# Kernel optimization log

Measured on AMD Instinct MI355X. Metric: run time of the kernel, lower is better.

The kernel has to match this reference:

```python
import jax, jax.numpy as jnp
import numpy as np
import math

N_HEADS = 32
N_KV_HEADS = 8
HEAD_DIM = 64
THETA = 10000.0
NEG_INF = -1e9


def _rope_cos_sin(seq_len, dim, dtype=jnp.float32):
    # freqs over even indices, matching torch.arange(0, dim, 2)/dim
    freqs = 1.0 / (THETA ** (jnp.arange(0, dim, 2, dtype=jnp.float32) / dim))  # [dim/2]
    angles = jnp.arange(seq_len, dtype=jnp.float32)[:, None] * freqs[None, :]  # [S, dim/2]
    return jnp.cos(angles).astype(dtype), jnp.sin(angles).astype(dtype)


def _apply_rope(x, cos, sin):
    # x: [B, S, H, D]; pairs (x[...,2i], x[...,2i+1]) rotated as complex numbers
    xr = x[..., 0::2]
    xi = x[..., 1::2]
    # broadcast cos/sin [S, D/2] -> [1, S, 1, D/2]
    c = cos[None, :, None, :]
    s = sin[None, :, None, :]
    or_ = xr * c - xi * s
    oi_ = xr * s + xi * c
    # interleave back: [..., D/2, 2] -> [..., D]
    return jnp.stack([or_, oi_], axis=-1).reshape(x.shape)


def setup_inputs() -> dict:
    key = jax.random.key(0)
    ks = jax.random.split(key, 5)
    B, S, D = 2, 2048, 2048
    KV_D = N_KV_HEADS * HEAD_DIM
    x = jax.random.normal(ks[0], (B, S, D), dtype=jnp.float32)
    sc = 1.0 / math.sqrt(D)
    wq = jax.random.normal(ks[1], (D, D), dtype=jnp.float32) * sc
    wk = jax.random.normal(ks[2], (D, KV_D), dtype=jnp.float32) * sc
    wv = jax.random.normal(ks[3], (D, KV_D), dtype=jnp.float32) * sc
    wo = jax.random.normal(ks[4], (D, D), dtype=jnp.float32) * sc
    # additive causal mask [1, 1, S, S]
    causal = jnp.tril(jnp.ones((S, S), dtype=bool))
    mask = jnp.where(causal, 0.0, NEG_INF).astype(jnp.float32)[None, None]
    return {"x": x, "mask": mask, "wq": wq, "wk": wk, "wv": wv, "wo": wo}


def reference(x, mask, wq, wk, wv, wo):
    B, S, D = x.shape
    n_rep = N_HEADS // N_KV_HEADS
    q = (x @ wq).reshape(B, S, N_HEADS, HEAD_DIM)
    k = (x @ wk).reshape(B, S, N_KV_HEADS, HEAD_DIM)
    v = (x @ wv).reshape(B, S, N_KV_HEADS, HEAD_DIM)
    cos, sin = _rope_cos_sin(S, HEAD_DIM)
    q = _apply_rope(q, cos, sin)
    k = _apply_rope(k, cos, sin)
    # GQA: repeat_interleave kv heads along head dim
    k = jnp.repeat(k, n_rep, axis=2)  # [B, S, H, D]
    v = jnp.repeat(v, n_rep, axis=2)
    scores = jnp.einsum("bqhd,bkhd->bhqk", q, k) / math.sqrt(HEAD_DIM)
    scores = scores + mask
    probs = jax.nn.softmax(scores.astype(jnp.float32), axis=-1).astype(q.dtype)
    out = jnp.einsum("bhqk,bkhd->bqhd", probs, v).reshape(B, S, N_HEADS * HEAD_DIM)
    return out @ wo
```

## Files before the change

### kernel.cpp

```cpp
#include <hip/hip_runtime.h>
#include <hip/hip_bf16.h>


#define S_LEN 2048
#define BATCH 2
#define D_MODEL 2048
#define NH 32
#define NKV 8
#define HD 64
#define KV_D (NKV * HD)
#define QKV_N (D_MODEL + 2 * KV_D)

typedef __attribute__((ext_vector_type(8))) short short8;
typedef __attribute__((ext_vector_type(4))) float float4v;

typedef __attribute__((address_space(1))) const unsigned int gu32;
typedef __attribute__((address_space(3))) unsigned int lu32;

#if __has_builtin(__builtin_amdgcn_exp2f)
#define PEXP(x) __builtin_amdgcn_exp2f(x)
#else
#define PEXP(x) __expf((x) * 0.69314718f)
#endif
#define QSCALE 0.18033688f

__device__ __forceinline__ float bf2f(unsigned short u) {
    unsigned x = ((unsigned)u) << 16;
    return __builtin_bit_cast(float, x);
}
__device__ __forceinline__ unsigned short f2bf(float f) {
    unsigned u = __builtin_bit_cast(unsigned, f);
    unsigned r = (u + 0x7fffu + ((u >> 16) & 1u)) >> 16;
    return (unsigned short)r;
}
__device__ __forceinline__ unsigned short f2bf_fast(float f) {
    return (unsigned short)((__builtin_bit_cast(unsigned, f) + 0x8000u) >> 16);
}

__global__ void cast_f32_bf16(const float* __restrict__ in,
                              unsigned short* __restrict__ out, long n) {
    long i = ((long)blockIdx.x * 256 + threadIdx.x) * 4;
    if (i + 3 >= n) return;
    const float4v v = *(const float4v*)&in[i];
    unsigned short o[4];
    o[0] = f2bf(v[0]); o[1] = f2bf(v[1]); o[2] = f2bf(v[2]); o[3] = f2bf(v[3]);
    *(__attribute__((ext_vector_type(4))) short*)&out[i] =
        *(__attribute__((ext_vector_type(4))) short*)o;
}

__global__ __launch_bounds__(256) void wtrans(const float* __restrict__ in,
                                              unsigned short* __restrict__ out,
                                              int K, int N) {
    __shared__ unsigned short t[32 * 33];
    const int nb = blockIdx.x * 32, kb = blockIdx.y * 32;
    const int c = threadIdx.x & 31, rr = threadIdx.x >> 5;
#pragma unroll
    for (int it = 0; it < 4; ++it) {
        int r = it * 8 + rr;
        t[c * 33 + r] = f2bf(in[(long)(kb + r) * N + nb + c]);
    }
    __syncthreads();
#pragma unroll
    for (int it = 0; it < 4; ++it) {
        int r = it * 8 + rr;
        out[(long)(nb + r) * K + kb + c] = t[r * 33 + c];
    }
}

template <int TM, bool F32OUT>
__global__ __launch_bounds__(256, TM == 64 ? 4 : 3)
void gemm_sw(const unsigned short* __restrict__ A,
             const unsigned short* __restrict__ BT,
             void* __restrict__ Cv, int M, int N, int K) {
    __shared__ unsigned short As[TM * 64];
    __shared__ unsigned short Bs[128 * 64];
    const int tid = threadIdx.x;
    const int wid = tid >> 6, lane = tid & 63;
    const int l15 = lane & 15, quad = lane >> 4;
    const int wm = (wid >> 1) * (TM / 2), wn = (wid & 1) * 64;
    const int row0 = blockIdx.x * TM, col0 = blockIdx.y * 128;
    constexpr int MI = TM / 32;

    float4v acc[MI][4];
    float4v z;
    z[0] = z[1] = z[2] = z[3] = 0.0f;
    for (int mi = 0; mi < MI; ++mi)
        for (int ni = 0; ni < 4; ++ni) acc[mi][ni] = z;

    const int r_ld = lane >> 3;
    const int swz_ld = ((lane & 7) ^ (lane >> 3)) * 8;
    const int sw = l15 & 7;

    for (int kb = 0; kb < K; kb += 64) {
        __syncthreads();
#pragma unroll
        for (int c = 0; c < 4; ++c) {
            int chunk = c * 4 + wid;
            int r = chunk * 8 + r_ld;
            __builtin_amdgcn_global_load_lds(
                (gu32*)&BT[(long)(col0 + r) * K + kb + swz_ld],
                (lu32*)&Bs[chunk * 512], 16, 0, 0);
            if (c < MI)
                __builtin_amdgcn_global_load_lds(
                    (gu32*)&A[(long)(row0 + r) * K + kb + swz_ld],
                    (lu32*)&As[chunk * 512], 16, 0, 0);
        }
        __syncthreads();
#pragma unroll
        for (int kk = 0; kk < 64; kk += 32) {
            short8 af[MI], bf[4];
#pragma unroll
            for (int i = 0; i < MI; ++i)
                af[i] = *(const short8*)
                    &As[(wm + i * 16 + l15) * 64 + ((((kk >> 3) + quad) ^ sw) << 3)];
#pragma unroll
            for (int i = 0; i < 4; ++i)
                bf[i] = *(const short8*)
                    &Bs[(wn + i * 16 + l15) * 64 + ((((kk >> 3) + quad) ^ sw) << 3)];
#pragma unroll
            for (int mi = 0; mi < MI; ++mi)
#pragma unroll
                for (int ni = 0; ni < 4; ++ni)
                    acc[mi][ni] = __builtin_amdgcn_mfma_f32_16x16x32_bf16(
                        af[mi], bf[ni], acc[mi][ni], 0, 0, 0);
        }
    }
#pragma unroll
    for (int mi = 0; mi < MI; ++mi)
#pragma unroll
        for (int ni = 0; ni < 4; ++ni)
#pragma unroll
            for (int r = 0; r < 4; ++r) {
                int m = row0 + wm + mi * 16 + quad * 4 + r;
                int n = col0 + wn + ni * 16 + l15;
                if (F32OUT)
                    ((float*)Cv)[(long)m * N + n] = acc[mi][ni][r];
                else
                    ((unsigned short*)Cv)[(long)m * N + n] = f2bf(acc[mi][ni][r]);
            }
}

__global__ __launch_bounds__(256) void rope2(unsigned short* __restrict__ qkv) {
    const int i = threadIdx.x & 31;
    const int row = blockIdx.x * 8 + (threadIdx.x >> 5);
    const int s = row & (S_LEN - 1);
    float freq = __expf(-0.28782313f * (float)i);
    float ang = (float)s * freq;
    float c = cosf(ang), sn = sinf(ang);
    unsigned* p = (unsigned*)qkv + ((long)row * QKV_N + 2 * i) / 2;
#pragma unroll
    for (int head = 0; head < 40; ++head) {
        const float qs = (head < 32) ? QSCALE : 1.0f;
        unsigned v = p[head * 32];
        float xr = bf2f((unsigned short)(v & 0xffff));
        float xi = bf2f((unsigned short)(v >> 16));
        unsigned short lo = f2bf((xr * c - xi * sn) * qs);
        unsigned short hi = f2bf((xr * sn + xi * c) * qs);
        p[head * 32] = (unsigned)lo | ((unsigned)hi << 16);
    }
}

__global__ __launch_bounds__(256) void vtrans(const unsigned short* __restrict__ qkv,
                                              unsigned short* __restrict__ Vt) {
    __shared__ unsigned t[64 * 33];
    const int st = blockIdx.x * 64, kh = blockIdx.y, b = blockIdx.z;
    const int tid = threadIdx.x;
    {
        const int r2 = tid >> 3, dbase = (tid & 7) * 8;
        const unsigned short* src =
            qkv + ((long)(b * S_LEN + st + 2 * r2)) * QKV_N + D_MODEL + KV_D + kh * HD + dbase;
        short8 lo = *(const short8*)src;
        short8 hi = *(const short8*)(src + QKV_N);
#pragma unroll
        for (int j = 0; j < 8; ++j)
            t[(dbase + j) * 33 + r2] =
                (unsigned)(unsigned short)lo[j] | ((unsigned)(unsigned short)hi[j] << 16);
    }
    __syncthreads();
    {
        const int d = tid >> 2, sb = (tid & 3) * 8;
        unsigned short o[16];
#pragma unroll
        for (int jj = 0; jj < 8; ++jj) {
            unsigned v = t[d * 33 + sb + jj];
            o[2 * jj] = (unsigned short)(v & 0xffff);
            o[2 * jj + 1] = (unsigned short)(v >> 16);
        }
        unsigned short* dst =
            Vt + ((long)((b * 8 + kh) * 64 + d)) * S_LEN + st + sb * 2;
        *(short8*)dst = *(short8*)&o[0];
        *(short8*)(dst + 8) = *(short8*)&o[8];
    }
}

__global__ __launch_bounds__(512, 4) void flash5(const unsigned short* __restrict__ qkv,
                                                 const unsigned short* __restrict__ Vt,
                                                 unsigned short* __restrict__ O) {
    __shared__ unsigned short Ks[2][64 * 64];
    __shared__ unsigned short Vs[2][64 * 64];
    __shared__ unsigned short Ps[8][16 * 72];

    const int tid = threadIdx.x, w = tid >> 6, lane = tid & 63;
    const int l15 = lane & 15, quad = lane >> 4;
    const int h = blockIdx.y, b = blockIdx.z;
    const int kh = h >> 2, bkh = b * 8 + kh;
    const int qtA = blockIdx.x;

    const int r_loc = lane >> 3;
    const int row_g = w * 8 + r_loc;
    const int swz_c = ((lane & 7) ^ r_loc) * 8;
    const unsigned short* Kg =
        qkv + (long)b * S_LEN * QKV_N + D_MODEL + kh * HD + swz_c;
    const unsigned short* Vg = Vt + ((long)bkh * 64 + row_g) * S_LEN + swz_c;
    const int sw = l15 & 7;

    float4v z;
    z[0] = z[1] = z[2] = z[3] = 0.0f;

    for (int tsel = 0; tsel < 2; ++tsel) {
        const int qt = tsel ? (15 - qtA) : qtA;
        const int m0 = qt * 128;
        const int row_w = m0 + w * 16;

        short8 aq[2];
        {
            const long qrow = ((long)(b * S_LEN) + row_w + l15) * QKV_N + h * HD;
            aq[0] = *(const short8*)&qkv[qrow + quad * 8];
            aq[1] = *(const short8*)&qkv[qrow + 32 + quad * 8];
        }

        float4v oacc[4];
        float lp[4];
#pragma unroll
        for (int nt = 0; nt < 4; ++nt) oacc[nt] = z;
#pragma unroll
        for (int r = 0; r < 4; ++r) lp[r] = 0.0f;

        const int nkt = 2 * qt + 2;

        __builtin_amdgcn_global_load_lds((gu32*)&Kg[(long)row_g * QKV_N],
                                         (lu32*)&Ks[0][w * 512], 16, 0, 0);
        __builtin_amdgcn_global_load_lds((gu32*)&Vg[0],
                                         (lu32*)&Vs[0][w * 512], 16, 0, 0);
        __syncthreads();

        for (int kti = 0; kti < nkt; ++kti) {
            const int k0 = kti * 64;
            const int cur = kti & 1;

            if (kti + 1 < nkt) {
                __builtin_amdgcn_global_load_lds(
                    (gu32*)&Kg[(long)(k0 + 64 + row_g) * QKV_N],
                    (lu32*)&Ks[cur ^ 1][w * 512], 16, 0, 0);
                __builtin_amdgcn_global_load_lds(
                    (gu32*)&Vg[k0 + 64],
                    (lu32*)&Vs[cur ^ 1][w * 512], 16, 0, 0);
            }

            if (row_w + 15 >= k0) {
                const bool maskband = (kti >= 2 * qt);

#pragma unroll
                for (int nt = 0; nt < 4; ++nt) {
                    const int rb = (nt * 16 + l15) * 64;
                    short8 bk0 = *(const short8*)&Ks[cur][rb + ((quad ^ sw) << 3)];
                    short8 bk1 = *(const short8*)&Ks[cur][rb + (((quad + 4) ^ sw) << 3)];
                    __builtin_amdgcn_s_setprio(1);
                    float4v s = __builtin_amdgcn_mfma_f32_16x16x32_bf16(aq[0], bk0, z, 0, 0, 0);
                    s = __builtin_amdgcn_mfma_f32_16x16x32_bf16(aq[1], bk1, s, 0, 0, 0);
                    __builtin_amdgcn_s_setprio(0);
#pragma unroll
                    for (int r = 0; r < 4; ++r) {
                        const int qidx = row_w + quad * 4 + r;
                        float v = s[r];
                        if (maskband && (k0 + nt * 16 + l15 > qidx)) v = -1e4f;
                        float p = PEXP(v);
                        lp[r] += p;
                        Ps[w][(quad * 4 + r) * 72 + nt * 16 + l15] = f2bf_fast(p);
                    }
                }

                short8 ap0 = *(const short8*)&Ps[w][l15 * 72 + quad * 8];
                short8 ap1 = *(const short8*)&Ps[w][l15 * 72 + 32 + quad * 8];
                __builtin_amdgcn_s_setprio(1);
#pragma unroll
                for (int nt = 0; nt < 4; ++nt) {
                    const int rb = (nt * 16 + l15) * 64;
                    short8 bv0 = *(const short8*)&Vs[cur][rb + ((quad ^ sw) << 3)];
                    short8 bv1 = *(const short8*)&Vs[cur][rb + (((quad + 4) ^ sw) << 3)];
                    oacc[nt] = __builtin_amdgcn_mfma_f32_16x16x32_bf16(ap0, bv0, oacc[nt], 0, 0, 0);
                    oacc[nt] = __builtin_amdgcn_mfma_f32_16x16x32_bf16(ap1, bv1, oacc[nt], 0, 0, 0);
                }
                __builtin_amdgcn_s_setprio(0);
            }
            __syncthreads();
        }

#pragma unroll
        for (int r = 0; r < 4; ++r) {
            float l = lp[r];
#pragma unroll
            for (int off = 1; off < 16; off <<= 1) l += __shfl_xor(l, off);
            float inv = 1.0f / l;
            int m = row_w + quad * 4 + r;
            long orow = ((long)(b * S_LEN) + m) * D_MODEL + h * HD;
#pragma unroll
            for (int nt = 0; nt < 4; ++nt)
                O[orow + nt * 16 + l15] = f2bf(oacc[nt][r] * inv);
        }
    }
}

extern "C" void kernel_launch(void* const* d_in, const int* in_sizes, int n_in,
                              void* d_out, int out_size, void* d_ws, size_t ws_size,
                              hipStream_t stream) {
    const float* x  = (const float*)d_in[0];
    const float* wq = (const float*)d_in[n_in - 4];
    const float* wk = (const float*)d_in[n_in - 3];
    const float* wv = (const float*)d_in[n_in - 2];
    const float* wo = (const float*)d_in[n_in - 1];
    float* out = (float*)d_out;

    unsigned short* ws    = (unsigned short*)d_ws;
    unsigned short* xb    = ws;
    unsigned short* Obuf  = ws;
    unsigned short* qkv   = xb + (long)BATCH * S_LEN * D_MODEL;
    unsigned short* woT   = qkv + (long)BATCH * S_LEN * QKV_N;
    unsigned short* wqkvT = woT + (long)D_MODEL * D_MODEL;
    unsigned short* Vt    = wqkvT;

    const int M = BATCH * S_LEN;
    const long xn = (long)M * D_MODEL;

    cast_f32_bf16<<<(int)(xn / 4 / 256), 256, 0, stream>>>(x, xb, xn);

    wtrans<<<dim3(D_MODEL / 32, D_MODEL / 32), 256, 0, stream>>>(wq, wqkvT, D_MODEL, D_MODEL);
    wtrans<<<dim3(KV_D / 32, D_MODEL / 32), 256, 0, stream>>>(wk, wqkvT + (long)D_MODEL * D_MODEL, D_MODEL, KV_D);
    wtrans<<<dim3(KV_D / 32, D_MODEL / 32), 256, 0, stream>>>(wv, wqkvT + (long)(D_MODEL + KV_D) * D_MODEL, D_MODEL, KV_D);
    wtrans<<<dim3(D_MODEL / 32, D_MODEL / 32), 256, 0, stream>>>(wo, woT, D_MODEL, D_MODEL);

    gemm_sw<128, false><<<dim3(M / 128, QKV_N / 128), 256, 0, stream>>>(
        xb, wqkvT, qkv, M, QKV_N, D_MODEL);

    rope2<<<M / 8, 256, 0, stream>>>(qkv);

    vtrans<<<dim3(S_LEN / 64, NKV, BATCH), 256, 0, stream>>>(qkv, Vt);

    flash5<<<dim3(8, NH, BATCH), 512, 0, stream>>>(qkv, Vt, Obuf);

    gemm_sw<64, true><<<dim3(M / 64, D_MODEL / 128), 256, 0, stream>>>(
        Obuf, woT, out, M, D_MODEL, D_MODEL);
}
```

Baseline: 313.2 us.

## Rewrite attention kernel with 32x32 MFMA and register-resident P

Replaces the flash attention kernel with a 4-wave variant that uses 32x32x16 bf16 MFMA. It computes S^T so the probabilities stay in registers and are repacked with cvt_pk_bf16 and permlane32 swaps, which removes the LDS round-trip for P. Each block now handles one query tile picked by a fixed permutation table, instead of pairing tiles for causal balance, and the grid doubles. The output is staged through LDS for coalesced 16-byte stores. It relies on gfx950-specific instructions and adds more accumulator register pressure.

```diff
diff --git a/kernel.cpp b/kernel.cpp
--- a/kernel.cpp
+++ b/kernel.cpp
@@ -13,6 +13,8 @@
 
 typedef __attribute__((ext_vector_type(8))) short short8;
 typedef __attribute__((ext_vector_type(4))) float float4v;
+typedef __attribute__((ext_vector_type(16))) float f32x16;
+typedef __attribute__((ext_vector_type(2))) unsigned uint2v;
 
 typedef __attribute__((address_space(1))) const unsigned int gu32;
 typedef __attribute__((address_space(3))) unsigned int lu32;
@@ -33,8 +35,26 @@
     unsigned r = (u + 0x7fffu + ((u >> 16) & 1u)) >> 16;
     return (unsigned short)r;
 }
-__device__ __forceinline__ unsigned short f2bf_fast(float f) {
-    return (unsigned short)((__builtin_bit_cast(unsigned, f) + 0x8000u) >> 16);
+
+__device__ __forceinline__ unsigned cvt_pk_bf16(float a, float b) {
+    unsigned r;
+    asm("v_cvt_pk_bf16_f32 %0, %1, %2" : "=v"(r) : "v"(a), "v"(b));
+    return r;
+}
+
+__device__ __forceinline__ void pl32swap(unsigned a, unsigned b,
+                                         unsigned& x, unsigned& y) {
+#if __has_builtin(__builtin_amdgcn_permlane32_swap)
+    uint2v r = __builtin_amdgcn_permlane32_swap(a, b, false, false);
+    x = r[0];
+    y = r[1];
+#else
+    unsigned pa = (unsigned)__shfl_xor((int)a, 32);
+    unsigned pb = (unsigned)__shfl_xor((int)b, 32);
+    bool lo = (threadIdx.x & 63) < 32;
+    x = lo ? a : pb;
+    y = lo ? pa : b;
+#endif
 }
 
 __global__ void cast_f32_bf16(const float* __restrict__ in,
@@ -193,122 +213,139 @@
     }
 }
 
-__global__ __launch_bounds__(512, 4) void flash5(const unsigned short* __restrict__ qkv,
+__global__ __launch_bounds__(256, 4) void flash6(const unsigned short* __restrict__ qkv,
                                                  const unsigned short* __restrict__ Vt,
                                                  unsigned short* __restrict__ O) {
     __shared__ unsigned short Ks[2][64 * 64];
     __shared__ unsigned short Vs[2][64 * 64];
-    __shared__ unsigned short Ps[8][16 * 72];
 
     const int tid = threadIdx.x, w = tid >> 6, lane = tid & 63;
-    const int l15 = lane & 15, quad = lane >> 4;
+    const int l31 = lane & 31, hi = lane >> 5;
+    const int r7 = l31 & 7;
     const int h = blockIdx.y, b = blockIdx.z;
     const int kh = h >> 2, bkh = b * 8 + kh;
-    const int qtA = blockIdx.x;
-
-    const int r_loc = lane >> 3;
-    const int row_g = w * 8 + r_loc;
-    const int swz_c = ((lane & 7) ^ r_loc) * 8;
+
+    const unsigned bx = blockIdx.x;
+    const int qt = (int)(((bx < 8) ? (0x97C2B5E0u >> (4 * bx))
+                                   : (0x683D4A1Fu >> (4 * (bx - 8)))) & 15u);
+    const int row_w = qt * 128 + w * 32;
+    const int nkt = 2 * qt + 2;
+
+    const int sr = lane >> 3;
+    const int sc = ((lane & 7) ^ sr) * 8;
+    const int kr0 = w * 8 + sr, kr1 = 32 + w * 8 + sr;
     const unsigned short* Kg =
-        qkv + (long)b * S_LEN * QKV_N + D_MODEL + kh * HD + swz_c;
-    const unsigned short* Vg = Vt + ((long)bkh * 64 + row_g) * S_LEN + swz_c;
-    const int sw = l15 & 7;
-
-    float4v z;
-    z[0] = z[1] = z[2] = z[3] = 0.0f;
-
-    for (int tsel = 0; tsel < 2; ++tsel) {
-        const int qt = tsel ? (15 - qtA) : qtA;
-        const int m0 = qt * 128;
-        const int row_w = m0 + w * 16;
-
-        short8 aq[2];
-        {
-            const long qrow = ((long)(b * S_LEN) + row_w + l15) * QKV_N + h * HD;
-            aq[0] = *(const short8*)&qkv[qrow + quad * 8];
-            aq[1] = *(const short8*)&qkv[qrow + 32 + quad * 8];
-        }
-
-        float4v oacc[4];
-        float lp[4];
-#pragma unroll
-        for (int nt = 0; nt < 4; ++nt) oacc[nt] = z;
-#pragma unroll
-        for (int r = 0; r < 4; ++r) lp[r] = 0.0f;
-
-        const int nkt = 2 * qt + 2;
-
-        __builtin_amdgcn_global_load_lds((gu32*)&Kg[(long)row_g * QKV_N],
-                                         (lu32*)&Ks[0][w * 512], 16, 0, 0);
-        __builtin_amdgcn_global_load_lds((gu32*)&Vg[0],
-                                         (lu32*)&Vs[0][w * 512], 16, 0, 0);
+        qkv + (long)b * S_LEN * QKV_N + D_MODEL + kh * HD + sc;
+    const unsigned short* Vg = Vt + ((long)bkh * 64) * S_LEN + sc;
+
+#define STAGE6(buf, kb)                                                              \
+    do {                                                                             \
+        __builtin_amdgcn_global_load_lds((gu32*)&Kg[(long)((kb) + kr0) * QKV_N],     \
+                                         (lu32*)&Ks[buf][w * 512], 16, 0, 0);        \
+        __builtin_amdgcn_global_load_lds((gu32*)&Kg[(long)((kb) + kr1) * QKV_N],     \
+                                         (lu32*)&Ks[buf][2048 + w * 512], 16, 0, 0); \
+        __builtin_amdgcn_global_load_lds((gu32*)&Vg[(long)kr0 * S_LEN + (kb)],       \
+                                         (lu32*)&Vs[buf][w * 512], 16, 0, 0);        \
+        __builtin_amdgcn_global_load_lds((gu32*)&Vg[(long)kr1 * S_LEN + (kb)],       \
+                                         (lu32*)&Vs[buf][2048 + w * 512], 16, 0, 0); \
+    } while (0)
+
+    short8 aq[4];
+    {
+        const long qbase = ((long)(b * S_LEN) + row_w + l31) * QKV_N + h * HD + hi * 8;
+#pragma unroll
+        for (int ks = 0; ks < 4; ++ks) aq[ks] = *(const short8*)&qkv[qbase + ks * 16];
+    }
+
+    f32x16 oacc[2] = {};
+    float lp = 0.0f;
+
+    STAGE6(0, 0);
+    __syncthreads();
+
+    for (int kti = 0; kti < nkt; ++kti) {
+        const int k0 = kti * 64;
+        const int cur = kti & 1;
+        if (kti + 1 < nkt) STAGE6(cur ^ 1, k0 + 64);
+
+        if (row_w + 31 >= k0) {
+            const bool mb = (k0 + 63 > row_w);
+#pragma unroll
+            for (int kb2 = 0; kb2 < 2; ++kb2) {
+                short8 kf[4];
+#pragma unroll
+                for (int ks = 0; ks < 4; ++ks)
+                    kf[ks] = *(const short8*)
+                        &Ks[cur][(kb2 * 32 + l31) * 64 + (((ks * 2 + hi) ^ r7) << 3)];
+                f32x16 s = {};
+                __builtin_amdgcn_s_setprio(1);
+#pragma unroll
+                for (int ks = 0; ks < 4; ++ks)
+                    s = __builtin_amdgcn_mfma_f32_32x32x16_bf16(kf[ks], aq[ks], s, 0, 0, 0);
+                __builtin_amdgcn_s_setprio(0);
+
+                const int qrel = row_w + l31 - k0 - kb2 * 32 - 4 * hi;
+#pragma unroll
+                for (int r = 0; r < 16; ++r) {
+                    float v = s[r];
+                    if (mb && ((r & 3) + 8 * (r >> 2) > qrel)) v = -1e4f;
+                    float p = PEXP(v);
+                    lp += p;
+                    s[r] = p;
+                }
+
+#pragma unroll
+                for (int ksl = 0; ksl < 2; ++ksl) {
+                    const int g = ksl * 8;
+                    unsigned ca = cvt_pk_bf16(s[g + 0], s[g + 1]);
+                    unsigned cb = cvt_pk_bf16(s[g + 2], s[g + 3]);
+                    unsigned cc = cvt_pk_bf16(s[g + 4], s[g + 5]);
+                    unsigned cd = cvt_pk_bf16(s[g + 6], s[g + 7]);
+                    unsigned dw0, dw1, dw2, dw3;
+                    pl32swap(ca, cc, dw0, dw2);
+                    pl32swap(cb, cd, dw1, dw3);
+                    union { unsigned u[4]; short8 v8; } pf;
+                    pf.u[0] = dw0; pf.u[1] = dw1; pf.u[2] = dw2; pf.u[3] = dw3;
+                    const int lc = kb2 * 4 + ksl * 2 + hi;
+                    __builtin_amdgcn_s_setprio(1);
+#pragma unroll
+                    for (int dblk = 0; dblk < 2; ++dblk) {
+                        short8 vf = *(const short8*)
+                            &Vs[cur][(dblk * 32 + l31) * 64 + ((lc ^ r7) << 3)];
+                        oacc[dblk] = __builtin_amdgcn_mfma_f32_32x32x16_bf16(
+                            vf, pf.v8, oacc[dblk], 0, 0, 0);
+                    }
+                    __builtin_amdgcn_s_setprio(0);
+                }
+            }
+        }
         __syncthreads();
-
-        for (int kti = 0; kti < nkt; ++kti) {
-            const int k0 = kti * 64;
-            const int cur = kti & 1;
-
-            if (kti + 1 < nkt) {
-                __builtin_amdgcn_global_load_lds(
-                    (gu32*)&Kg[(long)(k0 + 64 + row_g) * QKV_N],
-                    (lu32*)&Ks[cur ^ 1][w * 512], 16, 0, 0);
-                __builtin_amdgcn_global_load_lds(
-                    (gu32*)&Vg[k0 + 64],
-                    (lu32*)&Vs[cur ^ 1][w * 512], 16, 0, 0);
-            }
-
-            if (row_w + 15 >= k0) {
-                const bool maskband = (kti >= 2 * qt);
-
-#pragma unroll
-                for (int nt = 0; nt < 4; ++nt) {
-                    const int rb = (nt * 16 + l15) * 64;
-                    short8 bk0 = *(const short8*)&Ks[cur][rb + ((quad ^ sw) << 3)];
-                    short8 bk1 = *(const short8*)&Ks[cur][rb + (((quad + 4) ^ sw) << 3)];
-                    __builtin_amdgcn_s_setprio(1);
-                    float4v s = __builtin_amdgcn_mfma_f32_16x16x32_bf16(aq[0], bk0, z, 0, 0, 0);
-                    s = __builtin_amdgcn_mfma_f32_16x16x32_bf16(aq[1], bk1, s, 0, 0, 0);
-                    __builtin_amdgcn_s_setprio(0);
-#pragma unroll
-                    for (int r = 0; r < 4; ++r) {
-                        const int qidx = row_w + quad * 4 + r;
-                        float v = s[r];
-                        if (maskband && (k0 + nt * 16 + l15 > qidx)) v = -1e4f;
-                        float p = PEXP(v);
-                        lp[r] += p;
-                        Ps[w][(quad * 4 + r) * 72 + nt * 16 + l15] = f2bf_fast(p);
-                    }
-                }
-
-                short8 ap0 = *(const short8*)&Ps[w][l15 * 72 + quad * 8];
-                short8 ap1 = *(const short8*)&Ps[w][l15 * 72 + 32 + quad * 8];
-                __builtin_amdgcn_s_setprio(1);
-#pragma unroll
-                for (int nt = 0; nt < 4; ++nt) {
-                    const int rb = (nt * 16 + l15) * 64;
-                    short8 bv0 = *(const short8*)&Vs[cur][rb + ((quad ^ sw) << 3)];
-                    short8 bv1 = *(const short8*)&Vs[cur][rb + (((quad + 4) ^ sw) << 3)];
-                    oacc[nt] = __builtin_amdgcn_mfma_f32_16x16x32_bf16(ap0, bv0, oacc[nt], 0, 0, 0);
-                    oacc[nt] = __builtin_amdgcn_mfma_f32_16x16x32_bf16(ap1, bv1, oacc[nt], 0, 0, 0);
-                }
-                __builtin_amdgcn_s_setprio(0);
-            }
-            __syncthreads();
-        }
-
-#pragma unroll
-        for (int r = 0; r < 4; ++r) {
-            float l = lp[r];
-#pragma unroll
-            for (int off = 1; off < 16; off <<= 1) l += __shfl_xor(l, off);
-            float inv = 1.0f / l;
-            int m = row_w + quad * 4 + r;
-            long orow = ((long)(b * S_LEN) + m) * D_MODEL + h * HD;
-#pragma unroll
-            for (int nt = 0; nt < 4; ++nt)
-                O[orow + nt * 16 + l15] = f2bf(oacc[nt][r] * inv);
-        }
-    }
+    }
+
+    float linv = 1.0f / (lp + __shfl_xor(lp, 32));
+    unsigned short* Oe = &Ks[0][0] + w * 2048;
+#pragma unroll
+    for (int dblk = 0; dblk < 2; ++dblk)
+#pragma unroll
+        for (int rq = 0; rq < 4; ++rq) {
+            unsigned plo = cvt_pk_bf16(oacc[dblk][rq * 4 + 0] * linv,
+                                       oacc[dblk][rq * 4 + 1] * linv);
+            unsigned phi = cvt_pk_bf16(oacc[dblk][rq * 4 + 2] * linv,
+                                       oacc[dblk][rq * 4 + 3] * linv);
+            uint2v wv;
+            wv[0] = plo; wv[1] = phi;
+            int e = l31 * 64 + (((rq + 4 * dblk) ^ r7) << 3) + hi * 4;
+            *(uint2v*)&Oe[e] = wv;
+        }
+#pragma unroll
+    for (int i = 0; i < 4; ++i) {
+        int q2 = i * 8 + (lane >> 3);
+        int e = q2 * 64 + (((lane & 7) ^ (lane >> 3)) << 3);
+        short8 ov = *(const short8*)&Oe[e];
+        long orow = ((long)(b * S_LEN) + row_w + q2) * D_MODEL + h * HD + (lane & 7) * 8;
+        *(short8*)&O[orow] = ov;
+    }
+#undef STAGE6
 }
 
 extern "C" void kernel_launch(void* const* d_in, const int* in_sizes, int n_in,
@@ -346,7 +383,7 @@
 
     vtrans<<<dim3(S_LEN / 64, NKV, BATCH), 256, 0, stream>>>(qkv, Vt);
 
-    flash5<<<dim3(8, NH, BATCH), 512, 0, stream>>>(qkv, Vt, Obuf);
+    flash6<<<dim3(16, NH, BATCH), 256, 0, stream>>>(qkv, Vt, Obuf);
 
     gemm_sw<64, true><<<dim3(M / 64, D_MODEL / 128), 256, 0, stream>>>(
         Obuf, woT, out, M, D_MODEL, D_MODEL);
```

New measurement: 334.1 us. 6.7% more time.
